# Kernel optimization log

Hardware: AMD Instinct MI355X
Metric: run time of the kernel (lower is better)

## Reference

```python
import jax, jax.numpy as jnp
import numpy as np

B, N, C, W = 128, 512, 128, 128
MASK_FILL = -1e-06  # faithful to original (sic: -1e-06, not -1e6)


def setup_inputs() -> dict:
    key = jax.random.key(0)
    ks = jax.random.split(key, 8)
    s = 1.0 / np.sqrt(C)
    return {
        "x": jax.random.normal(ks[0], (B, N, C), dtype=jnp.float32),
        "Wq": jax.random.normal(ks[1], (C, W), dtype=jnp.float32) * s,
        "bq": jnp.zeros((W,), dtype=jnp.float32),
        "Wk": jax.random.normal(ks[2], (C, W), dtype=jnp.float32) * s,
        "bk": jnp.zeros((W,), dtype=jnp.float32),
        "Wv": jax.random.normal(ks[3], (C, W), dtype=jnp.float32) * s,
        "bv": jnp.zeros((W,), dtype=jnp.float32),
        "valid_len": jax.random.randint(ks[4], (B,), 0, N, dtype=jnp.int64),
    }


def reference(x, Wq, bq, Wk, bk, Wv, bv, valid_len):
    # QKV projections: [B, N, W]
    q = jnp.einsum("bnc,cw->bnw", x, Wq) + bq
    k = jnp.einsum("bnc,cw->bnw", x, Wk) + bk
    v = jnp.einsum("bnc,cw->bnw", x, Wv) + bv
    # scores: [B, N, N]
    scores = jnp.einsum("bnw,bmw->bnm", q, k)
    # masked softmax: positions m where m > valid_len[b] get MASK_FILL
    # (mask is identical across query rows n since valid_len is per-batch)
    keep = jnp.arange(N)[None, None, :] <= valid_len[:, None, None]  # [B,1,N]
    scores = jnp.where(keep, scores, MASK_FILL)
    attn = jax.nn.softmax(scores, axis=-1)
    return jnp.einsum("bnm,bmw->bnw", attn, v)
```

## Files before the change

### kernel.cpp

```cpp
#include <hip/hip_runtime.h>
#include <hip/hip_fp16.h>
#include <math.h>

#define B_ 128
#define N_ 512
#define C_ 128
#define W_ 128
#define LDSW 136

typedef _Float16 f16;
typedef _Float16 f16x8 __attribute__((ext_vector_type(8)));
typedef _Float16 f16x4 __attribute__((ext_vector_type(4)));
typedef float f32x4 __attribute__((ext_vector_type(4)));

#define MFMA16(a, b, c) __builtin_amdgcn_mfma_f32_16x16x32_f16(a, b, c, 0, 0, 0)

#define LOG2E 1.44269504f
#define MASKF (-1e-6f * LOG2E)

__global__ __launch_bounds__(256) void prep_w(const float* __restrict__ Wq,
                                              const float* __restrict__ Wk,
                                              const float* __restrict__ Wv,
                                              f16* __restrict__ wT) {
  __shared__ float xs[16 * 129];
  const float* src = blockIdx.x == 0 ? Wq : (blockIdx.x == 1 ? Wk : Wv);
  f16* dst = wT + (size_t)blockIdx.x * C_ * W_;
  const int c0 = blockIdx.y * 16;
  const int t = threadIdx.x;
  for (int ii = 0; ii < 2; ++ii) {
    int idx = t + 256 * ii;
    int row = idx >> 5, w4 = idx & 31;
    float4 v = *reinterpret_cast<const float4*>(src + (c0 + row) * W_ + w4 * 4);
    xs[row * 129 + w4 * 4 + 0] = v.x;
    xs[row * 129 + w4 * 4 + 1] = v.y;
    xs[row * 129 + w4 * 4 + 2] = v.z;
    xs[row * 129 + w4 * 4 + 3] = v.w;
  }
  __syncthreads();
  int o = t * 8;
  int w = o >> 4, cc = o & 15;
  f16x8 h;
  for (int jj = 0; jj < 8; ++jj) h[jj] = (f16)xs[(cc + jj) * 129 + w];
  *reinterpret_cast<f16x8*>(dst + w * C_ + c0 + cc) = h;
}

__global__ __launch_bounds__(256, 2) void proj(const float* __restrict__ x,
                                               const float* __restrict__ bq,
                                               const float* __restrict__ bk,
                                               const float* __restrict__ bv,
                                               const f16* __restrict__ wT,
                                               f16* __restrict__ q,
                                               f16* __restrict__ k,
                                               f16* __restrict__ vT) {
  __shared__ f16 wls[2][128 * LDSW];
  const int b = blockIdx.y, n0 = blockIdx.x * 128;
  const int t = threadIdx.x, wave = t >> 6, lane = t & 63;
  const int quad = lane >> 4, l15 = lane & 15;
  const int srow = t >> 4, sc16 = t & 15;

  float4 xr[2][4][2];
  for (int tile = 0; tile < 2; ++tile)
    for (int ks = 0; ks < 4; ++ks) {
      const float* p = x + ((size_t)(b * N_ + n0 + wave * 32 + tile * 16 +
                                     l15)) * C_ + ks * 32 + quad * 8;
      xr[tile][ks][0] = *reinterpret_cast<const float4*>(p);
      xr[tile][ks][1] = *reinterpret_cast<const float4*>(p + 4);
    }

  for (int i = 0; i < 8; ++i) {
    int idx = t + 256 * i;
    f16x8 tmp = *reinterpret_cast<const f16x8*>(wT + (size_t)idx * 8);
    *reinterpret_cast<f16x8*>(&wls[0][(idx >> 4) * LDSW + (idx & 15) * 8]) =
        tmp;
  }

  f16x8 af[2][4];
  for (int tile = 0; tile < 2; ++tile)
    for (int ks = 0; ks < 4; ++ks) {
      f16x8 h;
      h[0] = (f16)xr[tile][ks][0].x; h[1] = (f16)xr[tile][ks][0].y;
      h[2] = (f16)xr[tile][ks][0].z; h[3] = (f16)xr[tile][ks][0].w;
      h[4] = (f16)xr[tile][ks][1].x; h[5] = (f16)xr[tile][ks][1].y;
      h[6] = (f16)xr[tile][ks][1].z; h[7] = (f16)xr[tile][ks][1].w;
      af[tile][ks] = h;
    }
  __syncthreads();

  for (int ph = 0; ph < 3; ++ph) {
    const f16* wl = wls[ph & 1];

    f16x8 wst[8];
    if (ph < 2)
      for (int i = 0; i < 8; ++i)
        wst[i] = *reinterpret_cast<const f16x8*>(
            wT + (size_t)(ph + 1) * 16384 + (size_t)(t + 256 * i) * 8);

    f32x4 acc[8][2];
    for (int ct = 0; ct < 8; ++ct) {
      acc[ct][0] = {0.f, 0.f, 0.f, 0.f};
      acc[ct][1] = {0.f, 0.f, 0.f, 0.f};
    }

    if (ph < 2) {
      for (int ct = 0; ct < 8; ++ct) {
        f16x8 wf[4];
        for (int ks = 0; ks < 4; ++ks)
          wf[ks] = *reinterpret_cast<const f16x8*>(
              &wl[(ct * 16 + l15) * LDSW + ks * 32 + quad * 8]);
        for (int ks = 0; ks < 4; ++ks) {
          acc[ct][0] = MFMA16(wf[ks], af[0][ks], acc[ct][0]);
          acc[ct][1] = MFMA16(wf[ks], af[1][ks], acc[ct][1]);
        }
      }
      const float* bias = ph == 0 ? bq : bk;
      const float scale = ph == 0 ? LOG2E : 1.0f;
      f16* dst = ph == 0 ? q : k;
      for (int ct = 0; ct < 8; ++ct) {
        const float4 bb =
            *reinterpret_cast<const float4*>(bias + ct * 16 + quad * 4);
        for (int tile = 0; tile < 2; ++tile) {
          int n = n0 + wave * 32 + tile * 16 + l15;
          f16x4 h;
          h.x = (f16)((acc[ct][tile][0] + bb.x) * scale);
          h.y = (f16)((acc[ct][tile][1] + bb.y) * scale);
          h.z = (f16)((acc[ct][tile][2] + bb.z) * scale);
          h.w = (f16)((acc[ct][tile][3] + bb.w) * scale);
          *reinterpret_cast<f16x4*>(dst + ((size_t)(b * N_ + n)) * W_ +
                                    ct * 16 + quad * 4) = h;
        }
      }
    } else {
      for (int ct = 0; ct < 8; ++ct) {
        f16x8 wf[4];
        for (int ks = 0; ks < 4; ++ks)
          wf[ks] = *reinterpret_cast<const f16x8*>(
              &wl[(ct * 16 + l15) * LDSW + ks * 32 + quad * 8]);
        for (int ks = 0; ks < 4; ++ks) {
          acc[ct][0] = MFMA16(af[0][ks], wf[ks], acc[ct][0]);
          acc[ct][1] = MFMA16(af[1][ks], wf[ks], acc[ct][1]);
        }
      }
      for (int ct = 0; ct < 8; ++ct) {
        int wcol = ct * 16 + l15;
        float bb = bv[wcol];
        for (int tile = 0; tile < 2; ++tile) {
          int n = n0 + wave * 32 + tile * 16 + quad * 4;
          f16x4 h;
          h.x = (f16)(acc[ct][tile][0] + bb);
          h.y = (f16)(acc[ct][tile][1] + bb);
          h.z = (f16)(acc[ct][tile][2] + bb);
          h.w = (f16)(acc[ct][tile][3] + bb);
          *reinterpret_cast<f16x4*>(&vT[((size_t)(b * W_ + wcol)) * N_ + n]) =
              h;
        }
      }
    }

    if (ph < 2) {
      for (int i = 0; i < 8; ++i) {
        int idx = t + 256 * i;
        *reinterpret_cast<f16x8*>(
            &wls[(ph + 1) & 1][(idx >> 4) * LDSW + (idx & 15) * 8]) = wst[i];
      }
      __syncthreads();
    }
  }
}

__global__ __launch_bounds__(256, 2) void flash(const f16* __restrict__ q,
                                                const f16* __restrict__ k,
                                                const f16* __restrict__ vT,
                                                const int* __restrict__ vlen,
                                                float* __restrict__ out) {
  __shared__ f16 kls[128 * LDSW];
  __shared__ f16 pls[128 * LDSW];
  __shared__ float bcast[128];
  const int b = blockIdx.x, m0 = blockIdx.y * 128;
  const int t = threadIdx.x, wave = t >> 6, lane = t & 63;
  const int quad = lane >> 4, l15 = lane & 15;
  const int vl = vlen[b];
  const int mcol = m0 + wave * 32;
  const int srow = t >> 4, sc16 = t & 15;

  f16x8 qf[2][4];
  for (int ct = 0; ct < 2; ++ct)
    for (int kt = 0; kt < 4; ++kt)
      qf[ct][kt] = *reinterpret_cast<const f16x8*>(
          q + ((size_t)(b * N_ + mcol + ct * 16 + l15)) * W_ + kt * 32 +
          quad * 8);

  f32x4 oacc[2][8];
  for (int wt = 0; wt < 2; ++wt)
    for (int cm = 0; cm < 8; ++cm) oacc[wt][cm] = {0.f, 0.f, 0.f, 0.f};
  float mrun[2] = {-3.4e38f, -3.4e38f}, lrun[2] = {0.f, 0.f};

  for (int i = 0; i < 8; ++i) {
    int row = srow + 16 * i;
    f16x8 tmp = *reinterpret_cast<const f16x8*>(
        k + ((size_t)(b * N_ + row)) * W_ + sc16 * 8);
    *reinterpret_cast<f16x8*>(&kls[row * LDSW + sc16 * 8]) = tmp;
  }
  __syncthreads();

  for (int j = 0; j < 4; ++j) {
    const int n0 = j * 128;

    f16x8 kst[8];
    if (j < 3)
      for (int i = 0; i < 8; ++i)
        kst[i] = *reinterpret_cast<const f16x8*>(
            k + ((size_t)(b * N_ + n0 + 128 + srow + 16 * i)) * W_ + sc16 * 8);

    f32x4 sacc[8][2];
    for (int i = 0; i < 8; ++i) {
      sacc[i][0] = {0.f, 0.f, 0.f, 0.f};
      sacc[i][1] = {0.f, 0.f, 0.f, 0.f};
      f16x8 kf[4];
      for (int kt = 0; kt < 4; ++kt)
        kf[kt] = *reinterpret_cast<const f16x8*>(
            &kls[(i * 16 + l15) * LDSW + kt * 32 + quad * 8]);
      for (int kt = 0; kt < 4; ++kt) {
        sacc[i][0] = MFMA16(kf[kt], qf[0][kt], sacc[i][0]);
        sacc[i][1] = MFMA16(kf[kt], qf[1][kt], sacc[i][1]);
      }
    }

    for (int i = 0; i < 8; ++i)
      for (int r = 0; r < 4; ++r) {
        int n = n0 + 16 * i + quad * 4 + r;
        if (n > vl) { sacc[i][0][r] = MASKF; sacc[i][1][r] = MASKF; }
      }

    float alpha[2];
    for (int ct = 0; ct < 2; ++ct) {
      float mx = -3.4e38f;
      for (int i = 0; i < 8; ++i)
        for (int r = 0; r < 4; ++r) mx = fmaxf(mx, sacc[i][ct][r]);
      mx = fmaxf(mx, __shfl_xor(mx, 16));
      mx = fmaxf(mx, __shfl_xor(mx, 32));
      float mnew = fmaxf(mrun[ct], mx);
      alpha[ct] = exp2f(mrun[ct] - mnew);
      mrun[ct] = mnew;
      float s = 0.f;
      for (int i = 0; i < 8; ++i)
        for (int r = 0; r < 4; ++r) {
          float p = exp2f(sacc[i][ct][r] - mnew);
          sacc[i][ct][r] = p;
          s += p;
        }
      s += __shfl_xor(s, 16);
      s += __shfl_xor(s, 32);
      lrun[ct] = lrun[ct] * alpha[ct] + s;
    }

    for (int i = 0; i < 8; ++i)
      for (int ct = 0; ct < 2; ++ct) {
        f16x4 h;
        h.x = (f16)sacc[i][ct][0];
        h.y = (f16)sacc[i][ct][1];
        h.z = (f16)sacc[i][ct][2];
        h.w = (f16)sacc[i][ct][3];
        *reinterpret_cast<f16x4*>(
            &pls[(wave * 32 + ct * 16 + l15) * LDSW + 16 * i + quad * 4]) = h;
      }
    if (quad == 0) {
      bcast[wave * 32 + l15] = alpha[0];
      bcast[wave * 32 + 16 + l15] = alpha[1];
    }

    f16x8 vf[2][4];
    for (int wt = 0; wt < 2; ++wt)
      for (int kt = 0; kt < 4; ++kt)
        vf[wt][kt] = *reinterpret_cast<const f16x8*>(
            vT + ((size_t)(b * W_ + wave * 32 + wt * 16 + l15)) * N_ + n0 +
            kt * 32 + quad * 8);
    __syncthreads();

    if (j < 3)
      for (int i = 0; i < 8; ++i)
        *reinterpret_cast<f16x8*>(&kls[(srow + 16 * i) * LDSW + sc16 * 8]) =
            kst[i];

    float al[8];
    for (int cm = 0; cm < 8; ++cm) al[cm] = bcast[cm * 16 + l15];
    for (int wt = 0; wt < 2; ++wt)
      for (int cm = 0; cm < 8; ++cm) oacc[wt][cm] *= al[cm];
    for (int cm = 0; cm < 8; ++cm) {
      f16x8 pf[4];
      for (int kt = 0; kt < 4; ++kt)
        pf[kt] = *reinterpret_cast<const f16x8*>(
            &pls[(cm * 16 + l15) * LDSW + kt * 32 + quad * 8]);
      for (int kt = 0; kt < 4; ++kt) {
        oacc[0][cm] = MFMA16(vf[0][kt], pf[kt], oacc[0][cm]);
        oacc[1][cm] = MFMA16(vf[1][kt], pf[kt], oacc[1][cm]);
      }
    }
    __syncthreads();
  }

  if (quad == 0) {
    bcast[wave * 32 + l15] = 1.f / lrun[0];
    bcast[wave * 32 + 16 + l15] = 1.f / lrun[1];
  }
  __syncthreads();
  for (int cm = 0; cm < 8; ++cm) {
    float inv = bcast[cm * 16 + l15];
    int m = m0 + cm * 16 + l15;
    for (int wt = 0; wt < 2; ++wt) {
      int w = wave * 32 + wt * 16 + quad * 4;
      float4 o;
      o.x = oacc[wt][cm][0] * inv;
      o.y = oacc[wt][cm][1] * inv;
      o.z = oacc[wt][cm][2] * inv;
      o.w = oacc[wt][cm][3] * inv;
      *reinterpret_cast<float4*>(&out[((size_t)(b * N_ + m)) * W_ + w]) = o;
    }
  }
}

extern "C" void kernel_launch(void* const* d_in, const int* in_sizes, int n_in,
                              void* d_out, int out_size, void* d_ws,
                              size_t ws_size, hipStream_t stream) {
  const float* x  = (const float*)d_in[0];
  const float* Wq = (const float*)d_in[1];
  const float* bq = (const float*)d_in[2];
  const float* Wk = (const float*)d_in[3];
  const float* bk = (const float*)d_in[4];
  const float* Wv = (const float*)d_in[5];
  const float* bv = (const float*)d_in[6];
  const int* vlen = (const int*)d_in[7];
  float* out = (float*)d_out;

  char* ws = (char*)d_ws;
  f16* wT = (f16*)ws;
  f16* q  = (f16*)(ws + (1u << 20));
  f16* k  = (f16*)(ws + (1u << 20) + (16u << 20));
  f16* vT = (f16*)(ws + (1u << 20) + (32u << 20));

  prep_w<<<dim3(3, 8), 256, 0, stream>>>(Wq, Wk, Wv, wT);
  proj<<<dim3(4, 128), 256, 0, stream>>>(x, bq, bk, bv, wT, q, k, vT);
  flash<<<dim3(128, 4), 256, 0, stream>>>(q, k, vT, vlen, out);
}
```

Measured before the change: 141.8 us.

## Repartition PV product so each wave owns its query rows across all output columns

The P·V stage is re-split so each wave computes all 128 output columns for its own 32 query rows, rather than 32 output columns for all 128 rows. P stays wave-private in shared memory, which removes the alpha/1-over-l broadcast buffer and one block-wide barrier per tile, and drops barriers entirely on the last tile. The cost is that every wave now loads the full V tile from global memory (four times the V traffic per block). Register pressure also rises because of the larger accumulator and V fragment arrays.

```diff
diff --git a/kernel.cpp b/kernel.cpp
--- a/kernel.cpp
+++ b/kernel.cpp
@@ -56,7 +56,6 @@
   const int b = blockIdx.y, n0 = blockIdx.x * 128;
   const int t = threadIdx.x, wave = t >> 6, lane = t & 63;
   const int quad = lane >> 4, l15 = lane & 15;
-  const int srow = t >> 4, sc16 = t & 15;
 
   float4 xr[2][4][2];
   for (int tile = 0; tile < 2; ++tile)
@@ -174,7 +173,6 @@
                                                 float* __restrict__ out) {
   __shared__ f16 kls[128 * LDSW];
   __shared__ f16 pls[128 * LDSW];
-  __shared__ float bcast[128];
   const int b = blockIdx.x, m0 = blockIdx.y * 128;
   const int t = threadIdx.x, wave = t >> 6, lane = t & 63;
   const int quad = lane >> 4, l15 = lane & 15;
@@ -189,9 +187,9 @@
           q + ((size_t)(b * N_ + mcol + ct * 16 + l15)) * W_ + kt * 32 +
           quad * 8);
 
-  f32x4 oacc[2][8];
-  for (int wt = 0; wt < 2; ++wt)
-    for (int cm = 0; cm < 8; ++cm) oacc[wt][cm] = {0.f, 0.f, 0.f, 0.f};
+  f32x4 oacc[8][2];
+  for (int wt = 0; wt < 8; ++wt)
+    for (int ct = 0; ct < 2; ++ct) oacc[wt][ct] = {0.f, 0.f, 0.f, 0.f};
   float mrun[2] = {-3.4e38f, -3.4e38f}, lrun[2] = {0.f, 0.f};
 
   for (int i = 0; i < 8; ++i) {
@@ -201,6 +199,8 @@
     *reinterpret_cast<f16x8*>(&kls[row * LDSW + sc16 * 8]) = tmp;
   }
   __syncthreads();
+
+  f16* prow = &pls[(size_t)wave * 32 * LDSW];
 
   for (int j = 0; j < 4; ++j) {
     const int n0 = j * 128;
@@ -261,58 +261,62 @@
         h.z = (f16)sacc[i][ct][2];
         h.w = (f16)sacc[i][ct][3];
         *reinterpret_cast<f16x4*>(
-            &pls[(wave * 32 + ct * 16 + l15) * LDSW + 16 * i + quad * 4]) = h;
-      }
-    if (quad == 0) {
-      bcast[wave * 32 + l15] = alpha[0];
-      bcast[wave * 32 + 16 + l15] = alpha[1];
-    }
-
-    f16x8 vf[2][4];
-    for (int wt = 0; wt < 2; ++wt)
+            &prow[(ct * 16 + l15) * LDSW + 16 * i + quad * 4]) = h;
+      }
+
+    f16x8 vf[4][4];
+    for (int wt = 0; wt < 4; ++wt)
       for (int kt = 0; kt < 4; ++kt)
         vf[wt][kt] = *reinterpret_cast<const f16x8*>(
-            vT + ((size_t)(b * W_ + wave * 32 + wt * 16 + l15)) * N_ + n0 +
-            kt * 32 + quad * 8);
-    __syncthreads();
-
-    if (j < 3)
+            vT + ((size_t)(b * W_ + 16 * wt + l15)) * N_ + n0 + kt * 32 +
+            quad * 8);
+
+    if (j < 3) {
+      __syncthreads();
       for (int i = 0; i < 8; ++i)
         *reinterpret_cast<f16x8*>(&kls[(srow + 16 * i) * LDSW + sc16 * 8]) =
             kst[i];
-
-    float al[8];
-    for (int cm = 0; cm < 8; ++cm) al[cm] = bcast[cm * 16 + l15];
-    for (int wt = 0; wt < 2; ++wt)
-      for (int cm = 0; cm < 8; ++cm) oacc[wt][cm] *= al[cm];
-    for (int cm = 0; cm < 8; ++cm) {
-      f16x8 pf[4];
+      __syncthreads();
+    }
+
+    f16x8 pf[2][4];
+    for (int ct = 0; ct < 2; ++ct)
       for (int kt = 0; kt < 4; ++kt)
-        pf[kt] = *reinterpret_cast<const f16x8*>(
-            &pls[(cm * 16 + l15) * LDSW + kt * 32 + quad * 8]);
+        pf[ct][kt] = *reinterpret_cast<const f16x8*>(
+            &prow[(ct * 16 + l15) * LDSW + kt * 32 + quad * 8]);
+
+    for (int wt = 0; wt < 8; ++wt) {
+      oacc[wt][0] *= alpha[0];
+      oacc[wt][1] *= alpha[1];
+    }
+    for (int wt = 0; wt < 4; ++wt)
       for (int kt = 0; kt < 4; ++kt) {
-        oacc[0][cm] = MFMA16(vf[0][kt], pf[kt], oacc[0][cm]);
-        oacc[1][cm] = MFMA16(vf[1][kt], pf[kt], oacc[1][cm]);
-      }
-    }
-    __syncthreads();
-  }
-
-  if (quad == 0) {
-    bcast[wave * 32 + l15] = 1.f / lrun[0];
-    bcast[wave * 32 + 16 + l15] = 1.f / lrun[1];
-  }
-  __syncthreads();
-  for (int cm = 0; cm < 8; ++cm) {
-    float inv = bcast[cm * 16 + l15];
-    int m = m0 + cm * 16 + l15;
-    for (int wt = 0; wt < 2; ++wt) {
-      int w = wave * 32 + wt * 16 + quad * 4;
+        oacc[wt][0] = MFMA16(vf[wt][kt], pf[0][kt], oacc[wt][0]);
+        oacc[wt][1] = MFMA16(vf[wt][kt], pf[1][kt], oacc[wt][1]);
+      }
+
+    for (int wt = 0; wt < 4; ++wt)
+      for (int kt = 0; kt < 4; ++kt)
+        vf[wt][kt] = *reinterpret_cast<const f16x8*>(
+            vT + ((size_t)(b * W_ + 64 + 16 * wt + l15)) * N_ + n0 + kt * 32 +
+            quad * 8);
+    for (int wt = 0; wt < 4; ++wt)
+      for (int kt = 0; kt < 4; ++kt) {
+        oacc[4 + wt][0] = MFMA16(vf[wt][kt], pf[0][kt], oacc[4 + wt][0]);
+        oacc[4 + wt][1] = MFMA16(vf[wt][kt], pf[1][kt], oacc[4 + wt][1]);
+      }
+  }
+
+  for (int ct = 0; ct < 2; ++ct) {
+    float inv = 1.f / lrun[ct];
+    int m = mcol + ct * 16 + l15;
+    for (int wt = 0; wt < 8; ++wt) {
+      int w = 16 * wt + quad * 4;
       float4 o;
-      o.x = oacc[wt][cm][0] * inv;
-      o.y = oacc[wt][cm][1] * inv;
-      o.z = oacc[wt][cm][2] * inv;
-      o.w = oacc[wt][cm][3] * inv;
+      o.x = oacc[wt][ct][0] * inv;
+      o.y = oacc[wt][ct][1] * inv;
+      o.z = oacc[wt][ct][2] * inv;
+      o.w = oacc[wt][ct][3] * inv;
       *reinterpret_cast<float4*>(&out[((size_t)(b * N_ + m)) * W_ + w]) = o;
     }
   }
```

Measured after the change: 158.4 us. 11.7% more time.
